# Kernel optimization log

Measured on AMD Instinct MI355X. Metric: run time of the kernel, lower is better.

The kernel has to match this reference:

```python
import jax, jax.numpy as jnp
import numpy as np

EMBED_DIM = 512
B, N = 8, 2048


def setup_inputs() -> dict:
    key = jax.random.key(0)
    ks = jax.random.split(key, 9)
    d = EMBED_DIM
    s = 1.0 / np.sqrt(d)
    return {
        "x": jax.random.normal(ks[0], (B, N, d), dtype=jnp.float32),
        "Wq": jax.random.uniform(ks[1], (d, d), jnp.float32, -s, s),
        "bq": jax.random.uniform(ks[2], (d,), jnp.float32, -s, s),
        "Wk": jax.random.uniform(ks[3], (d, d), jnp.float32, -s, s),
        "bk": jax.random.uniform(ks[4], (d,), jnp.float32, -s, s),
        "Wv": jax.random.uniform(ks[5], (d, d), jnp.float32, -s, s),
        "bv": jax.random.uniform(ks[6], (d,), jnp.float32, -s, s),
        "Wo": jax.random.uniform(ks[7], (d, d), jnp.float32, -s, s),
        "bo": jax.random.uniform(ks[8], (d,), jnp.float32, -s, s),
    }


def reference(x, Wq, bq, Wk, bk, Wv, bv, Wo, bo):
    d = x.shape[-1]
    scale = d ** (-0.5)
    q = x @ Wq + bq              # [B, N, D]
    k = x @ Wk + bk
    v = x @ Wv + bv
    attn = jnp.einsum('bnd,bmd->bnm', q, k) * scale  # [B, N, N]
    attn = jax.nn.softmax(attn, axis=-1)
    out = jnp.einsum('bnm,bmd->bnd', attn, v)
    return out @ Wo + bo
```

## Files before the change

### kernel.cpp

```cpp
#include <hip/hip_runtime.h>
#include <hip/hip_bf16.h>
#include <hip/hip_fp8.h>
#include <stdint.h>

typedef __bf16 bf16;
typedef __attribute__((ext_vector_type(8))) short short8;
typedef __attribute__((ext_vector_type(4))) float f32x4;
typedef __attribute__((ext_vector_type(4))) bf16 bf16x4;
typedef __attribute__((ext_vector_type(8))) int int8v;
typedef __attribute__((ext_vector_type(4))) int int4v;

#define DIM 512
#define NBATCH 8
#define SEQ 2048

#define VMCNT(N) asm volatile("s_waitcnt vmcnt(" #N ")" ::: "memory")

__device__ __forceinline__ void gld_lds16(const void* g, void* l) {
    __builtin_amdgcn_global_load_lds(
        (const __attribute__((address_space(1))) void*)g,
        (__attribute__((address_space(3))) void*)l,
        16, 0, 0);
}

__device__ __forceinline__ unsigned char f32_to_e4m3(float v) {
#if __has_builtin(__builtin_amdgcn_cvt_pk_fp8_f32)
    return (unsigned char)(__builtin_amdgcn_cvt_pk_fp8_f32(v, v, 0, false) & 0xff);
#else
    return __hip_cvt_float_to_fp8(v, __HIP_SATFINITE, __HIP_E4M3);
#endif
}

template <int MODE, int SWIZ>
__global__ __launch_bounds__(256) void gemm_bt(
    const bf16* __restrict__ A, const bf16* __restrict__ Bt,
    void* __restrict__ Cv, uint8_t* __restrict__ Vt,
    const float* __restrict__ bias, int N, int K, int gx)
{
    __shared__ bf16 smem[32768];
    bf16* Asb = smem;
    bf16* Bsb = smem + 16384;

    int bx, by;
    {
        const unsigned g = blockIdx.x;
        const unsigned xcd = g & 7;
        const unsigned t = g >> 3;
        const unsigned per = (gridDim.x >> 3) / (unsigned)gx;
        by = xcd * per + t / (unsigned)gx;
        bx = t % (unsigned)gx;
    }

    const int tid  = threadIdx.x;
    const int lane = tid & 63;
    const int w    = tid >> 6;
    const int wr   = w >> 1;
    const int wc   = w & 1;
    const int lm   = lane & 15;
    const int lk   = lane >> 4;
    const int fs   = lm & 7;
    const int rq   = tid >> 3;
    const int pc   = tid & 7;
    const int scol = ((pc ^ (rq & 7)) * 8);

    const bf16* Ag = A + (size_t)(by * 128) * K;
    const bf16* Bg = Bt + (size_t)(bx * 128) * K;

    f32x4 acc[4][4];
#pragma unroll
    for (int i = 0; i < 4; ++i)
#pragma unroll
        for (int j = 0; j < 4; ++j)
            acc[i][j] = (f32x4){0.f, 0.f, 0.f, 0.f};

    auto stage = [&](int kb, int buf) {
#pragma unroll
        for (int t = 0; t < 4; ++t) {
            const int r = t * 32 + rq;
            gld_lds16(Ag + (size_t)r * K + kb + scol,
                      Asb + buf * 8192 + t * 2048 + tid * 8);
            gld_lds16(Bg + (size_t)r * K + kb + scol,
                      Bsb + buf * 8192 + t * 2048 + tid * 8);
        }
    };
    auto compute = [&](int buf) {
        const bf16* Ab = Asb + buf * 8192;
        const bf16* Bb = Bsb + buf * 8192;
#pragma unroll
        for (int s = 0; s < 2; ++s) {
            const int u = ((s * 4 + lk) ^ fs) * 8;
            short8 fa[4], fb[4];
#pragma unroll
            for (int i = 0; i < 4; ++i)
                fa[i] = *(const short8*)&Ab[(wr * 64 + i * 16 + lm) * 64 + u];
#pragma unroll
            for (int j = 0; j < 4; ++j)
                fb[j] = *(const short8*)&Bb[(wc * 64 + j * 16 + lm) * 64 + u];
#pragma unroll
            for (int i = 0; i < 4; ++i)
#pragma unroll
                for (int j = 0; j < 4; ++j)
                    acc[i][j] = __builtin_amdgcn_mfma_f32_16x16x32_bf16(
                        fa[i], fb[j], acc[i][j], 0, 0, 0);
        }
    };

    stage(0, 0);
    __syncthreads();
    const int E = K >> 6;
#pragma unroll 2
    for (int e = 0; e < E; ++e) {
        if (e + 1 < E) stage((e + 1) << 6, (e + 1) & 1);
        compute(e & 1);
        __syncthreads();
    }

#pragma unroll
    for (int i = 0; i < 4; ++i)
#pragma unroll
        for (int j = 0; j < 4; ++j) {
            const int col = bx * 128 + wc * 64 + j * 16 + lm;
            const float bv = bias[col];
#pragma unroll
            for (int r = 0; r < 4; ++r)
                acc[i][j][r] += bv;
        }

    if (MODE == 2) {
        float* ft = (float*)smem;
        float* outp = (float*)Cv;
#pragma unroll
        for (int h = 0; h < 2; ++h) {
            if (wr == h) {
#pragma unroll
                for (int i = 0; i < 4; ++i)
#pragma unroll
                    for (int j = 0; j < 4; ++j)
#pragma unroll
                        for (int r = 0; r < 4; ++r)
                            ft[(i * 16 + lk * 4 + r) * 132 + wc * 64 + j * 16 + lm] =
                                acc[i][j][r];
            }
            __syncthreads();
            const int rr = tid >> 5, cc = (tid & 31) * 4;
#pragma unroll
            for (int p = 0; p < 8; ++p) {
                const int row = p * 8 + rr;
                *(float4*)&outp[(size_t)(by * 128 + h * 64 + row) * N +
                                bx * 128 + cc] = *(const float4*)&ft[row * 132 + cc];
            }
            __syncthreads();
        }
        return;
    }

    const int sub  = (bx * 128) >> 9;
    const int col0 = (bx * 128) & 511;

    if (sub == 2) {
        const int b  = (by * 128) >> 11;
        const int n0 = (by * 128) & 2047;
        uint8_t* t8 = (uint8_t*)smem;
#pragma unroll
        for (int i = 0; i < 4; ++i)
#pragma unroll
            for (int j = 0; j < 4; ++j)
#pragma unroll
                for (int r = 0; r < 4; ++r) {
                    const int fl = wc * 64 + j * 16 + lm;
                    const int nl = wr * 64 + i * 16 + lk * 4 + r;
                    t8[fl * 144 + nl] = f32_to_e4m3(32.0f * acc[i][j][r]);
                }
        __syncthreads();
        const int f = tid >> 1, nh = (tid & 1) * 64;
#pragma unroll
        for (int p = 0; p < 4; ++p) {
            const uint4 raw = *(const uint4*)&t8[f * 144 + nh + p * 16];
            *(uint4*)&Vt[((size_t)(b * 512 + col0 + f)) * 2048 +
                         n0 + nh + p * 16] = raw;
        }
        return;
    }

    uint8_t* d8 = (uint8_t*)Cv + (size_t)sub * 8388608;
    uint8_t* t8 = (uint8_t*)smem;
#pragma unroll
    for (int h = 0; h < 2; ++h) {
        if (wr == h) {
#pragma unroll
            for (int i = 0; i < 4; ++i)
#pragma unroll
                for (int j = 0; j < 4; ++j)
#pragma unroll
                    for (int r = 0; r < 4; ++r)
                        t8[(i * 16 + lk * 4 + r) * 144 + wc * 64 + j * 16 + lm] =
                            f32_to_e4m3(32.0f * acc[i][j][r]);
        }
        __syncthreads();
        const int rr = tid >> 3, cc = (tid & 7) * 16;
#pragma unroll
        for (int p = 0; p < 2; ++p) {
            const int row = p * 32 + rr;
            const uint4 raw = *(const uint4*)&t8[row * 144 + cc];
            *(uint4*)&d8[(size_t)(by * 128 + h * 64 + row) * 512 + col0 + cc] =
                raw;
        }
        __syncthreads();
    }
}

template <int MODE, int E>
__global__ __launch_bounds__(256) void gemm_mx(
    const uint8_t* __restrict__ A, const uint8_t* __restrict__ Bt,
    void* __restrict__ Cv, float* __restrict__ rsum,
    int N, int K, long long sA, long long sB, long long sC, float alpha,
    int gx)
{
    __shared__ uint8_t smem[65536];
    uint8_t* Asb = smem;
    uint8_t* Bsb = smem + 32768;

    int bx, by, bz;
    {
        const unsigned g = blockIdx.x;
        bz = g & 7;
        const unsigned r = g >> 3;
        bx = r % (unsigned)gx;
        by = r / (unsigned)gx;
    }

    const int tid  = threadIdx.x;
    const int lane = tid & 63;
    const int w    = tid >> 6;
    const int wr   = w >> 1;
    const int wc   = w & 1;
    const int lm   = lane & 15;
    const int lk   = lane >> 4;
    const int rq   = tid >> 3;
    const int pc   = tid & 7;
    const int ssrc = (pc ^ (rq & 7)) * 16;
    const int ca   = ((2 * lk) ^ (lm & 7)) * 16;
    const int cb   = ((2 * lk + 1) ^ (lm & 7)) * 16;

    const size_t z = bz;
    const uint8_t* Ag = A + z * (size_t)sA + (size_t)(by * 128) * K;
    const uint8_t* Bg = Bt + z * (size_t)sB + (size_t)(bx * 128) * K;

    f32x4 acc[4][4];
#pragma unroll
    for (int i = 0; i < 4; ++i)
#pragma unroll
        for (int j = 0; j < 4; ++j)
            acc[i][j] = (f32x4){0.f, 0.f, 0.f, 0.f};

    auto stageA = [&](int kb, int buf) {
#pragma unroll
        for (int t = 0; t < 4; ++t) {
            const int r = t * 32 + rq;
            gld_lds16(Ag + (size_t)r * K + kb + ssrc,
                      Asb + buf * 16384 + t * 4096 + tid * 16);
        }
    };
    auto stageB02 = [&](int kb, int buf) {
#pragma unroll
        for (int t = 0; t < 4; t += 2) {
            const int r = t * 32 + rq;
            gld_lds16(Bg + (size_t)r * K + kb + ssrc,
                      Bsb + buf * 16384 + t * 4096 + tid * 16);
        }
    };
    auto stageB13 = [&](int kb, int buf) {
#pragma unroll
        for (int t = 1; t < 4; t += 2) {
            const int r = t * 32 + rq;
            gld_lds16(Bg + (size_t)r * K + kb + ssrc,
                      Bsb + buf * 16384 + t * 4096 + tid * 16);
        }
    };
    auto loadB = [&](const uint8_t* Bs, int j) -> int8v {
        const uint8_t* rp = Bs + (wc * 64 + j * 16 + lm) * 128;
        const int4v lo = *(const int4v*)(rp + ca);
        const int4v hi = *(const int4v*)(rp + cb);
        return (int8v){lo[0], lo[1], lo[2], lo[3], hi[0], hi[1], hi[2], hi[3]};
    };

    stageA(0, 0); stageB02(0, 0); stageB13(0, 0);

#pragma unroll
    for (int e = 0; e < E; ++e) {
        const int p = e & 1;
        const uint8_t* As = Asb + p * 16384;
        const uint8_t* Bs = Bsb + p * 16384;

        VMCNT(2);
        __builtin_amdgcn_s_barrier();
        if (e + 1 < E) {
            stageA((e + 1) * 128, p ^ 1);
            stageB02((e + 1) * 128, p ^ 1);
            stageB13((e + 1) * 128, p ^ 1);
        }
        int8v fa[4];
#pragma unroll
        for (int i = 0; i < 4; ++i) {
            const uint8_t* rp = As + (wr * 64 + i * 16 + lm) * 128;
            const int4v lo = *(const int4v*)(rp + ca);
            const int4v hi = *(const int4v*)(rp + cb);
            fa[i] = (int8v){lo[0], lo[1], lo[2], lo[3],
                            hi[0], hi[1], hi[2], hi[3]};
        }
        __builtin_amdgcn_s_setprio(1);
#pragma unroll
        for (int j = 0; j < 2; ++j) {
            const int8v fb = loadB(Bs, j);
#pragma unroll
            for (int i = 0; i < 4; ++i)
                acc[i][j] = __builtin_amdgcn_mfma_scale_f32_16x16x128_f8f6f4(
                    fa[i], fb, acc[i][j], 0, 0, 0, 127, 0, 127);
        }
        __builtin_amdgcn_s_setprio(0);

        if (e + 1 < E) { VMCNT(8); } else { VMCNT(0); }
        __builtin_amdgcn_s_barrier();
        __builtin_amdgcn_s_setprio(1);
#pragma unroll
        for (int j = 2; j < 4; ++j) {
            const int8v fb = loadB(Bs, j);
#pragma unroll
            for (int i = 0; i < 4; ++i)
                acc[i][j] = __builtin_amdgcn_mfma_scale_f32_16x16x128_f8f6f4(
                    fa[i], fb, acc[i][j], 0, 0, 0, 127, 0, 127);
        }
        __builtin_amdgcn_s_setprio(0);
    }
    __syncthreads();

    const int orow0 = by * 128 + wr * 64;

    if (MODE == 4) {
#pragma unroll
        for (int i = 0; i < 4; ++i) {
            float psum[4] = {0.f, 0.f, 0.f, 0.f};
#pragma unroll
            for (int j = 0; j < 4; ++j)
#pragma unroll
                for (int r = 0; r < 4; ++r) {
                    const float e = __expf(acc[i][j][r] * alpha);
                    acc[i][j][r] = e;
                    psum[r] += e;
                }
#pragma unroll
            for (int m = 1; m < 16; m <<= 1)
#pragma unroll
                for (int r = 0; r < 4; ++r) psum[r] += __shfl_xor(psum[r], m);
            if (lm == 0) {
#pragma unroll
                for (int r = 0; r < 4; ++r)
                    atomicAdd(&rsum[z * SEQ + orow0 + i * 16 + lk * 4 + r],
                              psum[r]);
            }
        }
        uint8_t* dst = (uint8_t*)Cv + z * (size_t)sC;
#pragma unroll
        for (int h = 0; h < 2; ++h) {
            if (wr == h) {
#pragma unroll
                for (int i = 0; i < 4; ++i)
#pragma unroll
                    for (int j = 0; j < 4; ++j)
#pragma unroll
                        for (int r = 0; r < 4; ++r)
                            smem[(i * 16 + lk * 4 + r) * 144 +
                                 wc * 64 + j * 16 + lm] =
                                f32_to_e4m3(acc[i][j][r]);
            }
            __syncthreads();
            const int rr = tid >> 3, cc = (tid & 7) * 16;
#pragma unroll
            for (int p = 0; p < 2; ++p) {
                const int row = p * 32 + rr;
                const uint4 raw = *(const uint4*)&smem[row * 144 + cc];
                *(uint4*)&dst[(size_t)(by * 128 + h * 64 + row) * N +
                              bx * 128 + cc] = raw;
            }
            __syncthreads();
        }
        return;
    }

#pragma unroll
    for (int i = 0; i < 4; ++i) {
        float inv[4];
#pragma unroll
        for (int r = 0; r < 4; ++r)
            inv[r] = 1.0f / (32.0f * rsum[z * SEQ + orow0 + i * 16 + lk * 4 + r]);
#pragma unroll
        for (int j = 0; j < 4; ++j)
#pragma unroll
            for (int r = 0; r < 4; ++r)
                acc[i][j][r] *= inv[r];
    }
    bf16* dst = (bf16*)Cv + z * (size_t)sC;
    bf16* tile = (bf16*)smem;
#pragma unroll
    for (int h = 0; h < 2; ++h) {
        if (wr == h) {
#pragma unroll
            for (int i = 0; i < 4; ++i)
#pragma unroll
                for (int j = 0; j < 4; ++j)
#pragma unroll
                    for (int r = 0; r < 4; ++r)
                        tile[(i * 16 + lk * 4 + r) * 136 + wc * 64 + j * 16 + lm] =
                            (bf16)acc[i][j][r];
        }
        __syncthreads();
        const int rr0 = tid >> 4, cc = (tid & 15) * 8;
#pragma unroll
        for (int p = 0; p < 4; ++p) {
            const int row = p * 16 + rr0;
            const uint4 raw = *(const uint4*)&tile[row * 136 + cc];
            *(uint4*)&dst[(size_t)(by * 128 + h * 64 + row) * N + bx * 128 + cc] =
                raw;
        }
        __syncthreads();
    }
}

__global__ __launch_bounds__(256) void cvt_f32_bf16(
    const float* __restrict__ x, bf16* __restrict__ o, int n4)
{
    const int i = blockIdx.x * 256 + threadIdx.x;
    if (i >= n4) return;
    const float4 v = ((const float4*)x)[i];
    bf16x4 b;
    b[0] = (bf16)v.x; b[1] = (bf16)v.y; b[2] = (bf16)v.z; b[3] = (bf16)v.w;
    ((bf16x4*)o)[i] = b;
}

__global__ __launch_bounds__(256) void transpose4(
    const float* __restrict__ Wq, const float* __restrict__ Wk,
    const float* __restrict__ Wv, const float* __restrict__ Wo,
    bf16* __restrict__ Wcat, bf16* __restrict__ Wto,
    const float* __restrict__ bq, const float* __restrict__ bk,
    const float* __restrict__ bv, float* __restrict__ bcat,
    float* __restrict__ rowsum)
{
    const int widx = blockIdx.z;
    const int t0 = threadIdx.x;
    if (widx == 4) {
        const int idx = (blockIdx.y * 8 + blockIdx.x) * 256 + t0;
        rowsum[idx] = 0.0f;
        if (idx < 1536)
            bcat[idx] = (idx < 512) ? bq[idx]
                      : (idx < 1024) ? bk[idx - 512] : bv[idx - 1024];
        return;
    }
    __shared__ bf16 tile[64][65];
    const float* W = (widx == 0) ? Wq : (widx == 1) ? Wk : (widx == 2) ? Wv : Wo;
    bf16* dst = (widx < 3) ? (Wcat + (size_t)widx * 512 * 512) : Wto;
    const int tx = blockIdx.x, ty = blockIdx.y;
#pragma unroll
    for (int it = 0; it < 16; ++it) {
        const int e = it * 256 + t0;
        const int r = e >> 6, c = e & 63;
        tile[r][c] = (bf16)W[(size_t)(ty * 64 + r) * 512 + tx * 64 + c];
    }
    __syncthreads();
#pragma unroll
    for (int it = 0; it < 16; ++it) {
        const int e = it * 256 + t0;
        const int o = e >> 6, i = e & 63;
        dst[(size_t)(tx * 64 + o) * 512 + ty * 64 + i] = tile[i][o];
    }
}

extern "C" void kernel_launch(void* const* d_in, const int* in_sizes, int n_in,
                              void* d_out, int out_size, void* d_ws, size_t ws_size,
                              hipStream_t stream)
{
    const float* x  = (const float*)d_in[0];
    const float* Wq = (const float*)d_in[1];
    const float* bq = (const float*)d_in[2];
    const float* Wk = (const float*)d_in[3];
    const float* bk = (const float*)d_in[4];
    const float* Wv = (const float*)d_in[5];
    const float* bv = (const float*)d_in[6];
    const float* Wo = (const float*)d_in[7];
    const float* bo = (const float*)d_in[8];
    float* out = (float*)d_out;

    char* ws = (char*)d_ws;
    bf16*    Xb     = (bf16*)(ws);
    bf16*    Ctx    = (bf16*)(ws);
    bf16*    Wcat   = (bf16*)(ws + 16777216);
    bf16*    Wto    = (bf16*)(ws + 18350080);
    float*   bcat   = (float*)(ws + 18874368);
    float*   rowsum = (float*)(ws + 18880512);
    uint8_t* Q8     = (uint8_t*)(ws + 20971520);
    uint8_t* K8     = (uint8_t*)(ws + 29360128);
    uint8_t* Vt8    = (uint8_t*)(ws + 54525952);
    uint8_t* S8     = (uint8_t*)(ws + 62914560);

    transpose4<<<dim3(8, 8, 5), 256, 0, stream>>>(
        Wq, Wk, Wv, Wo, Wcat, Wto, bq, bk, bv, bcat, rowsum);
    cvt_f32_bf16<<<8192, 256, 0, stream>>>(x, Xb, 2097152);

    const float scale = 0.044194173824159216f;

    gemm_bt<3, 2><<<1536, 256, 0, stream>>>(
        Xb, Wcat, Q8, Vt8, bcat, 1536, 512, 12);

    gemm_mx<4, 4><<<2048, 256, 0, stream>>>(
        Q8, K8, S8, rowsum, 2048, 512,
        2048LL * 512, 2048LL * 512, 2048LL * 2048, scale / 1024.0f, 16);

    gemm_mx<5, 16><<<512, 256, 0, stream>>>(
        S8, Vt8, Ctx, rowsum, 512, 2048,
        2048LL * 2048, 512LL * 2048, 2048LL * 512, 1.0f, 4);

    gemm_bt<2, 2><<<512, 256, 0, stream>>>(
        Ctx, Wto, out, nullptr, bo, 512, 512, 4);
}
```

Measured before the change: 215.5 us.

## Add dedicated 256x256-tile FP8 QK^T kernel with 512 threads

```diff
diff --git a/kernel.cpp b/kernel.cpp
--- a/kernel.cpp
+++ b/kernel.cpp
@@ -15,6 +15,7 @@
 #define SEQ 2048
 
 #define VMCNT(N) asm volatile("s_waitcnt vmcnt(" #N ")" ::: "memory")
+#define CFENCE   asm volatile("" ::: "memory")
 
 __device__ __forceinline__ void gld_lds16(const void* g, void* l) {
     __builtin_amdgcn_global_load_lds(
@@ -204,6 +205,149 @@
             const uint4 raw = *(const uint4*)&t8[row * 144 + cc];
             *(uint4*)&d8[(size_t)(by * 128 + h * 64 + row) * 512 + col0 + cc] =
                 raw;
+        }
+        __syncthreads();
+    }
+}
+
+__global__ __launch_bounds__(512) void gemm_qk(
+    const uint8_t* __restrict__ Q, const uint8_t* __restrict__ Kt,
+    uint8_t* __restrict__ S, float* __restrict__ rsum, float alpha)
+{
+    __shared__ uint8_t smem[131072];
+
+    int bx, by, bz;
+    {
+        const unsigned g = blockIdx.x;
+        bz = g & 7;
+        const unsigned r = g >> 3;
+        bx = r & 7;
+        by = r >> 3;
+    }
+
+    const int tid  = threadIdx.x;
+    const int lane = tid & 63;
+    const int w    = tid >> 6;
+    const int wr   = w >> 2;
+    const int wc   = w & 3;
+    const int lm   = lane & 15;
+    const int lk   = lane >> 4;
+    const int rq   = tid >> 3;
+    const int pc   = tid & 7;
+    const int ssrc = (pc ^ (rq & 7)) * 16;
+    const int ca   = ((2 * lk) ^ (lm & 7)) * 16;
+    const int cb   = ((2 * lk + 1) ^ (lm & 7)) * 16;
+
+    const size_t z = bz;
+    const uint8_t* Ag = Q + z * (size_t)(SEQ * DIM) + (size_t)(by * 256) * DIM;
+    const uint8_t* Bg = Kt + z * (size_t)(SEQ * DIM) + (size_t)(bx * 256) * DIM;
+
+    f32x4 acc[8][4];
+#pragma unroll
+    for (int i = 0; i < 8; ++i)
+#pragma unroll
+        for (int j = 0; j < 4; ++j)
+            acc[i][j] = (f32x4){0.f, 0.f, 0.f, 0.f};
+
+    auto stage = [&](int kb, int buf) {
+        uint8_t* Ad = smem + buf * 65536 + tid * 16;
+        uint8_t* Bd = smem + buf * 65536 + 32768 + tid * 16;
+#pragma unroll
+        for (int t = 0; t < 4; ++t) {
+            const int r = t * 64 + rq;
+            gld_lds16(Ag + (size_t)r * DIM + kb + ssrc, Ad + t * 8192);
+            gld_lds16(Bg + (size_t)r * DIM + kb + ssrc, Bd + t * 8192);
+        }
+    };
+
+    stage(0, 0);
+#pragma unroll
+    for (int e = 0; e < 4; ++e) {
+        const int p = e & 1;
+        CFENCE;
+        __builtin_amdgcn_s_barrier();
+        CFENCE;
+        if (e + 1 < 4) { stage((e + 1) * 128, p ^ 1); VMCNT(8); }
+        else           { VMCNT(0); }
+        CFENCE;
+        __builtin_amdgcn_s_barrier();
+        CFENCE;
+
+        const uint8_t* As = smem + p * 65536;
+        const uint8_t* Bs = smem + p * 65536 + 32768;
+        int8v fb[4];
+#pragma unroll
+        for (int j = 0; j < 4; ++j) {
+            const uint8_t* rp = Bs + (wc * 64 + j * 16 + lm) * 128;
+            const int4v lo = *(const int4v*)(rp + ca);
+            const int4v hi = *(const int4v*)(rp + cb);
+            fb[j] = (int8v){lo[0], lo[1], lo[2], lo[3],
+                            hi[0], hi[1], hi[2], hi[3]};
+        }
+        __builtin_amdgcn_s_setprio(1);
+#pragma unroll
+        for (int i = 0; i < 8; ++i) {
+            const uint8_t* rp = As + (wr * 128 + i * 16 + lm) * 128;
+            const int4v lo = *(const int4v*)(rp + ca);
+            const int4v hi = *(const int4v*)(rp + cb);
+            const int8v fa = (int8v){lo[0], lo[1], lo[2], lo[3],
+                                     hi[0], hi[1], hi[2], hi[3]};
+#pragma unroll
+            for (int j = 0; j < 4; ++j)
+                acc[i][j] = __builtin_amdgcn_mfma_scale_f32_16x16x128_f8f6f4(
+                    fa, fb[j], acc[i][j], 0, 0, 0, 127, 0, 127);
+        }
+        __builtin_amdgcn_s_setprio(0);
+    }
+    __syncthreads();
+
+    const int orow0 = by * 256 + wr * 128;
+
+#pragma unroll
+    for (int i = 0; i < 8; ++i) {
+        float psum[4] = {0.f, 0.f, 0.f, 0.f};
+#pragma unroll
+        for (int j = 0; j < 4; ++j)
+#pragma unroll
+            for (int r = 0; r < 4; ++r) {
+                const float e = __expf(acc[i][j][r] * alpha);
+                acc[i][j][r] = e;
+                psum[r] += e;
+            }
+#pragma unroll
+        for (int m = 1; m < 16; m <<= 1)
+#pragma unroll
+            for (int r = 0; r < 4; ++r) psum[r] += __shfl_xor(psum[r], m);
+        if (lm == 0) {
+#pragma unroll
+            for (int r = 0; r < 4; ++r)
+                atomicAdd(&rsum[z * SEQ + orow0 + i * 16 + lk * 4 + r],
+                          psum[r]);
+        }
+    }
+
+    uint8_t* dst = S + z * (size_t)SEQ * SEQ;
+#pragma unroll
+    for (int h = 0; h < 2; ++h) {
+        if (wr == h) {
+#pragma unroll
+            for (int i = 0; i < 8; ++i)
+#pragma unroll
+                for (int j = 0; j < 4; ++j)
+#pragma unroll
+                    for (int r = 0; r < 4; ++r)
+                        smem[(i * 16 + lk * 4 + r) * 272 +
+                             wc * 64 + j * 16 + lm] =
+                            f32_to_e4m3(acc[i][j][r]);
+        }
+        __syncthreads();
+        const int rr = tid >> 2, c0 = (tid & 3) * 16;
+#pragma unroll
+        for (int p = 0; p < 4; ++p) {
+            const int col = c0 + p * 64;
+            const uint4 raw = *(const uint4*)&smem[rr * 272 + col];
+            *(uint4*)&dst[(size_t)(by * 256 + h * 128 + rr) * SEQ +
+                          bx * 256 + col] = raw;
         }
         __syncthreads();
     }
@@ -510,9 +654,7 @@
     gemm_bt<3, 2><<<1536, 256, 0, stream>>>(
         Xb, Wcat, Q8, Vt8, bcat, 1536, 512, 12);
 
-    gemm_mx<4, 4><<<2048, 256, 0, stream>>>(
-        Q8, K8, S8, rowsum, 2048, 512,
-        2048LL * 512, 2048LL * 512, 2048LL * 2048, scale / 1024.0f, 16);
+    gemm_qk<<<512, 512, 0, stream>>>(Q8, K8, S8, rowsum, scale / 1024.0f);
 
     gemm_mx<5, 16><<<512, 256, 0, stream>>>(
         S8, Vt8, Ctx, rowsum, 512, 2048,
```

New measurement: 264.1 us. 1.23x slower.
